# Optimization experiments

Hardware: AMD Instinct MI355X
Metric: run time of the kernel (lower is better)

The kernel has to match this reference:

```python
import jax, jax.numpy as jnp
import numpy as np

N = 4096      # num nodes
E = 131072    # num edges
D = 128       # embed dim (in=out)
HID = 16      # kan hidden dim
G, K = 4, 3   # KAN grid_size / spline_order (GCN + FFN kans)
GA, KA = 2, 1 # attention KANLinear grid_size / spline_order
H, HD = 8, 16 # heads, head_dim

def make_grid(in_f, g, k):
    h = 2.0 / g
    pts = (np.arange(-k, g + k + 1) * h - 1.0).astype(np.float32)  # [g+2k+1]
    return jnp.asarray(np.tile(pts[None, :], (in_f, 1)))            # [in_f, g+2k+1]

GRID_D = make_grid(D, G, K)
GRID_H = make_grid(HID, G, K)
GRID_A = make_grid(D, GA, KA)

def b_splines(x, grid, k):
    # x: [n, in] -> B-spline bases [n, in, g+k] via Cox-de-Boor recursion
    x = x[:, :, None]
    g = grid[None]
    bases = ((x >= g[..., :-1]) & (x < g[..., 1:])).astype(x.dtype)
    for j in range(1, k + 1):
        bases = ((x - g[..., :-(j + 1)]) / (g[..., j:-1] - g[..., :-(j + 1)]) * bases[..., :-1]
                 + (g[..., j + 1:] - x) / (g[..., j + 1:] - g[..., 1:-j]) * bases[..., 1:])
    return bases

def kan_lin(x, bw, sw, grid, k, use_silu):
    base = jax.nn.silu(x) if use_silu else x
    return base @ bw.T + jnp.einsum('nig,oig->no', b_splines(x, grid, k), sw)

def ekan2(x, bw1, sw1, bw2, sw2):
    # eKAN with layers_hidden=[D, HID, D], SiLU base activation
    h = kan_lin(x, bw1, sw1, GRID_D, K, True)
    return kan_lin(h, bw2, sw2, GRID_H, K, True)

def layer_norm(h, s, b):
    m = jnp.mean(h, axis=-1, keepdims=True)
    v = jnp.var(h, axis=-1, keepdims=True)
    return (h - m) * jax.lax.rsqrt(v + 1e-5) * s + b

def setup_inputs() -> dict:
    key = jax.random.key(0)
    ks = jax.random.split(key, 20)
    r = lambda i, shape: jax.random.normal(ks[i], shape, jnp.float32) * 0.1
    return dict(
        x=jax.random.normal(ks[0], (N, D), jnp.float32),
        edge_index=jax.random.randint(ks[1], (2, E), 0, N),
        gcn_bw1=r(2, (HID, D)), gcn_sw1=r(3, (HID, D, G + K)),
        gcn_bw2=r(4, (D, HID)), gcn_sw2=r(5, (D, HID, G + K)),
        q_bw=r(6, (D, D)), q_sw=r(7, (D, D, GA + KA)),
        k_bw=r(8, (D, D)), k_sw=r(9, (D, D, GA + KA)),
        v_bw=r(10, (D, D)), v_sw=r(11, (D, D, GA + KA)),
        ffn_bw1=r(12, (HID, D)), ffn_sw1=r(13, (HID, D, G + K)),
        ffn_bw2=r(14, (D, HID)), ffn_sw2=r(15, (D, HID, G + K)),
        ln1_s=jnp.ones(D), ln1_b=jnp.zeros(D),
        ln2_s=jnp.ones(D), ln2_b=jnp.zeros(D),
        ln3_s=jnp.ones(D), ln3_b=jnp.zeros(D),
    )

def reference(x, edge_index, gcn_bw1, gcn_sw1, gcn_bw2, gcn_sw2,
              q_bw, q_sw, k_bw, k_sw, v_bw, v_sw,
              ffn_bw1, ffn_sw1, ffn_bw2, ffn_sw2,
              ln1_s, ln1_b, ln2_s, ln2_b, ln3_s, ln3_b):
    n = x.shape[0]
    # ---- local GCN-KAN branch: KAN(A_hat x) ----
    loops = jnp.arange(n)
    row = jnp.concatenate([edge_index[0], loops])  # sources (+ self-loops)
    col = jnp.concatenate([edge_index[1], loops])  # targets
    w = jnp.ones(row.shape[0], x.dtype)
    deg = jax.ops.segment_sum(w, row, num_segments=n)
    dis = jnp.where(deg > 0, deg ** -0.5, 0.0)
    norm = dis[row] * w * dis[col]
    agg = jax.ops.segment_sum(norm[:, None] * x[row], col, num_segments=n)  # [n, D]
    h_local = ekan2(agg, gcn_bw1, gcn_sw1, gcn_bw2, gcn_sw2)
    h_local = layer_norm(x + h_local, ln1_s, ln1_b)
    # ---- global KAN multi-head attention branch ----
    Q = kan_lin(x, q_bw, q_sw, GRID_A, KA, False).reshape(n, H, HD)
    Kv = kan_lin(x, k_bw, k_sw, GRID_A, KA, False).reshape(n, H, HD)
    V = kan_lin(x, v_bw, v_sw, GRID_A, KA, False).reshape(n, H, HD)
    scores = jnp.einsum('nhd,mhd->hnm', Q, Kv) / np.sqrt(HD)  # [H, n, n]
    attn = jax.nn.softmax(scores, axis=-1)
    h_attn = jnp.einsum('hnm,mhd->nhd', attn, V).reshape(n, D)
    h_attn = layer_norm(x + h_attn, ln2_s, ln2_b)
    # ---- combine + KAN feed-forward ----
    h = h_local + h_attn
    out = layer_norm(h + ekan2(h, ffn_bw1, ffn_sw1, ffn_bw2, ffn_sw2), ln3_s, ln3_b)
    return out
```

## Files before the change

### kernel.cpp

```cpp
#include <hip/hip_runtime.h>

typedef unsigned short u16;
typedef unsigned int u32;

#define D_ 128
#define HID_ 16
#define NH_ 8
#define HD_ 16
#define PSTRIDE 17

#define WE_W1G 0
#define WE_W2G 16384
#define WE_W1F 32768
#define WE_W2F 49152
#define WE_TOTAL 65536

#define KROW 24
#define VROW 136
#define PROW 40
#define HROW 136
#define AROW 1032
#define HVROW 132

#define QSCALE 0.3606737602222409f

typedef __attribute__((ext_vector_type(8))) short bfrag;
typedef __attribute__((ext_vector_type(4))) float ffrag;

#if defined(__has_builtin)
#if __has_builtin(__builtin_amdgcn_exp2f)
#define EXP2F(x) __builtin_amdgcn_exp2f(x)
#endif
#endif
#ifndef EXP2F
#define EXP2F(x) exp2f(x)
#endif


__device__ __forceinline__ float bf2f(u16 u) {
    union { u32 i; float f; } v; v.i = ((u32)u) << 16; return v.f;
}
__device__ __forceinline__ u16 f2bf(float f) {
    u32 x = __float_as_uint(f);
    u32 r = (x + 0x7fffu + ((x >> 16) & 1u)) >> 16;
    return (u16)r;
}
__device__ __forceinline__ float rdf(const void* p, int i, bool bf) {
    return bf ? bf2f(((const u16*)p)[i]) : ((const float*)p)[i];
}

__device__ __forceinline__ u32 probe_stat(const u16* p) {
    for (int i = 0; i < 128; i++) {
        u16 u = p[i];
        int e = (u >> 7) & 0xFF;
        int m = u & 0x7F;
        bool zero = (e == 0) && (m == 0);
        bool sane = zero || (e >= 97 && e <= 147);
        if (!sane) return 0u;
    }
    return 1u;
}

__global__ __launch_bounds__(256) void k_detect(const void* x,
                         const void* gbw1, const void* gsw1, const void* gbw2, const void* gsw2,
                         const void* qbw, const void* qsw, const void* kbw, const void* ksw,
                         const void* vbw, const void* vsw,
                         const void* fbw1, const void* fsw1, const void* fbw2, const void* fsw2,
                         const void* l1s, const void* l1b, const void* l2s, const void* l2b,
                         const void* l3s, const void* l3b,
                         u32* flags, int* __restrict__ cnt3, int N) {
    int t = threadIdx.x;
    const void* ptrs[21] = {x, gbw1, gsw1, gbw2, gsw2, qbw, qsw, kbw, ksw, vbw, vsw,
                            fbw1, fsw1, fbw2, fsw2, l1s, l1b, l2s, l2b, l3s, l3b};
    if (t < 21) {
        u32 f = 0;
        if (t == 15 || t == 17 || t == 19) {
            f = (((const u32*)ptrs[t])[0] != 0x3F800000u) ? 1u : 0u;
        } else if (t == 16 || t == 18 || t == 20) {
            f = 0;
        } else {
            f = probe_stat((const u16*)ptrs[t]);
        }
        flags[t] = f;
    }
    __syncthreads();
    if (t == 16 || t == 18 || t == 20) flags[t] = flags[t - 1];
    int tot = 3 * N;
    for (int i = t; i < tot; i += 256) cnt3[i] = 0;
}

__device__ __forceinline__ float cub_seg(float s) {
    if (s < 0.0f || s >= 4.0f) return 0.0f;
    if (s < 1.0f) return s * s * s * (1.0f / 6.0f);
    if (s < 2.0f) { float r = s - 1.0f; return (1.0f + 3.0f * r + 3.0f * r * r - 3.0f * r * r * r) * (1.0f / 6.0f); }
    if (s < 3.0f) { float r = s - 2.0f; return (4.0f - 6.0f * r * r + 3.0f * r * r * r) * (1.0f / 6.0f); }
    float q = 4.0f - s; return q * q * q * (1.0f / 6.0f);
}
__device__ __forceinline__ float lin_seg(float s) {
    if (s < 0.0f || s >= 2.0f) return 0.0f;
    return (s < 1.0f) ? s : (2.0f - s);
}

__device__ __forceinline__ uint4 feat8(float a) {
    float si = a / (1.0f + __expf(-a));
    float u = (a + 2.5f) * 2.0f;
    float b0 = cub_seg(u), b1 = cub_seg(u - 1.0f), b2 = cub_seg(u - 2.0f), b3 = cub_seg(u - 3.0f);
    float b4 = cub_seg(u - 4.0f), b5 = cub_seg(u - 5.0f), b6 = cub_seg(u - 6.0f);
    uint4 r;
    r.x = (u32)f2bf(si) | ((u32)f2bf(b0) << 16);
    r.y = (u32)f2bf(b1) | ((u32)f2bf(b2) << 16);
    r.z = (u32)f2bf(b3) | ((u32)f2bf(b4) << 16);
    r.w = (u32)f2bf(b5) | ((u32)f2bf(b6) << 16);
    return r;
}

__global__ __launch_bounds__(256) void k_setup(const void* __restrict__ x,
        const void* l1s, const void* l1b, const void* l2s,
        const void* l2b, const void* l3s, const void* l3b,
        const void* gbw1, const void* gsw1, const void* gbw2, const void* gsw2,
        const void* fbw1, const void* fsw1, const void* fbw2, const void* fsw2,
        const void* qbw, const void* qsw, const void* kbw, const void* ksw,
        const void* vbw, const void* vsw,
        const int* __restrict__ ei,
        const u32* __restrict__ flags,
        float* __restrict__ xin, float* __restrict__ lnp,
        u16* __restrict__ F,
        u16* __restrict__ Web, u16* __restrict__ Wb,
        int* __restrict__ cnt, int* __restrict__ degi,
        int N, int E) {
    int b = blockIdx.x;
    int convB = ((N * D_ + 768) + 255) >> 8;
    if (b < convB) {
        int i = b * 256 + threadIdx.x;
        if (i < N * D_) {
            float xv = rdf(x, i, flags[0] != 0);
            xin[i] = xv;
            float u = xv + 2.0f;
            u32 lo = (u32)f2bf(xv) | ((u32)f2bf(lin_seg(u)) << 16);
            u32 hi = (u32)f2bf(lin_seg(u - 1.0f)) | ((u32)f2bf(lin_seg(u - 2.0f)) << 16);
            ((uint2*)F)[i] = make_uint2(lo, hi);
        } else if (i < N * D_ + 768) {
            int j = i - N * D_;
            int sel = j >> 7, k = j & 127;
            const void* p = sel == 0 ? l1s : sel == 1 ? l1b : sel == 2 ? l2s
                         : sel == 3 ? l2b : sel == 4 ? l3s : l3b;
            lnp[j] = rdf(p, k, flags[15 + sel] != 0);
        }
    } else if (b < convB + 224) {
        int t = (b - convB) * 256 + threadIdx.x;
        if (t < 8192) {
            int seg = t >> 11, i = t & 2047;
            const void* bw = seg == 0 ? gbw1 : seg == 1 ? gbw2 : seg == 2 ? fbw1 : fbw2;
            const void* sw = seg == 0 ? gsw1 : seg == 1 ? gsw2 : seg == 2 ? fsw1 : fsw2;
            int fb = seg == 0 ? 1 : seg == 1 ? 3 : seg == 2 ? 11 : 13;
            bool bwbf = flags[fb] != 0, swbf = flags[fb + 1] != 0;
            u16* dst = Web + (size_t)seg * 16384 + (size_t)i * 8;
            dst[0] = f2bf(rdf(bw, i, bwbf));
#pragma unroll
            for (int g = 0; g < 7; g++) dst[1 + g] = f2bf(rdf(sw, i * 7 + g, swbf));
        } else if (t < 8192 + 49152) {
            int uu = t - 8192;
            int seg = uu >> 14, i = uu & 16383;
            const void* bw = seg == 0 ? qbw : seg == 1 ? kbw : vbw;
            const void* sw = seg == 0 ? qsw : seg == 1 ? ksw : vsw;
            int fb = 5 + seg * 2;
            bool bwbf = flags[fb] != 0, swbf = flags[fb + 1] != 0;
            float sc = (seg == 0) ? QSCALE : 1.0f;
            u16* dst = Wb + (size_t)seg * 65536 + (size_t)i * 4;
            dst[0] = f2bf(rdf(bw, i, bwbf) * sc);
#pragma unroll
            for (int g = 0; g < 3; g++) dst[1 + g] = f2bf(rdf(sw, i * 3 + g, swbf) * sc);
        }
    } else {
        int e = (b - convB - 224) * 256 + threadIdx.x;
        if (e < E) {
            atomicAdd(&degi[ei[e]], 1);
            atomicAdd(&cnt[ei[E + e]], 1);
        }
    }
}

__global__ __launch_bounds__(1024) void k_scan(const int* __restrict__ cnt,
                                               const int* __restrict__ degi,
                                               int* __restrict__ rowptr,
                                               float* __restrict__ dis, int N) {
    __shared__ int ws[16];
    int t = threadIdx.x;
    int base = t * 4;
    int a[4];
#pragma unroll
    for (int k = 0; k < 4; k++) a[k] = (base + k < N) ? cnt[base + k] : 0;
    int loc = a[0] + a[1] + a[2] + a[3];
    int pre = loc;
#pragma unroll
    for (int off = 1; off < 64; off <<= 1) {
        int v = __shfl_up(pre, off, 64);
        if ((t & 63) >= off) pre += v;
    }
    if ((t & 63) == 63) ws[t >> 6] = pre;
    __syncthreads();
    if (t < 64) {
        int v = (t < 16) ? ws[t] : 0;
#pragma unroll
        for (int off = 1; off < 16; off <<= 1) {
            int u = __shfl_up(v, off, 64);
            if (t >= off) v += u;
        }
        if (t < 16) ws[t] = v;
    }
    __syncthreads();
    int ex = pre - loc + ((t >= 64) ? ws[(t >> 6) - 1] : 0);
    int run = ex;
#pragma unroll
    for (int k = 0; k < 4; k++) {
        if (base + k < N) rowptr[base + k] = run;
        run += a[k];
    }
    if (t == 1023) rowptr[N] = ws[15];
#pragma unroll
    for (int k = 0; k < 4; k++)
        if (base + k < N) dis[base + k] = rsqrtf((float)degi[base + k] + 1.0f);
}

__global__ void k_fill(const int* __restrict__ ei, const int* __restrict__ rowptr,
                       int* __restrict__ fill, int* __restrict__ elist, int E) {
    int e = blockIdx.x * 256 + threadIdx.x;
    if (e < E) {
        int r = ei[e], c = ei[E + e];
        int pos = rowptr[c] + atomicAdd(&fill[c], 1);
        elist[pos] = r;
    }
}

#define EKAN_G1(W1B) \
    if (ww == 0) { \
        const u16* ar = hfA + (size_t)l15 * AROW + quad * 8; \
        const u16* br = (W1B) + (size_t)l15 * 1024 + quad * 8; \
        ffrag c0 = {0,0,0,0}, c1 = {0,0,0,0}, c2 = {0,0,0,0}, c3 = {0,0,0,0}; \
        for (int ks = 0; ks < 256; ks += 32) { \
            c0 = __builtin_amdgcn_mfma_f32_16x16x32_bf16(*(const bfrag*)(ar + ks),       *(const bfrag*)(br + ks),       c0, 0, 0, 0); \
            c1 = __builtin_amdgcn_mfma_f32_16x16x32_bf16(*(const bfrag*)(ar + 256 + ks), *(const bfrag*)(br + 256 + ks), c1, 0, 0, 0); \
            c2 = __builtin_amdgcn_mfma_f32_16x16x32_bf16(*(const bfrag*)(ar + 512 + ks), *(const bfrag*)(br + 512 + ks), c2, 0, 0, 0); \
            c3 = __builtin_amdgcn_mfma_f32_16x16x32_bf16(*(const bfrag*)(ar + 768 + ks), *(const bfrag*)(br + 768 + ks), c3, 0, 0, 0); \
        } \
        float e0 = (c0.x + c1.x) + (c2.x + c3.x); \
        float e1 = (c0.y + c1.y) + (c2.y + c3.y); \
        float e2 = (c0.z + c1.z) + (c2.z + c3.z); \
        float e3 = (c0.w + c1.w) + (c2.w + c3.w); \
        { uint4 fv = feat8(e0); *(uint4*)(&hfL[(quad * 4 + 0) * HROW + l15 * 8]) = fv; } \
        { uint4 fv = feat8(e1); *(uint4*)(&hfL[(quad * 4 + 1) * HROW + l15 * 8]) = fv; } \
        { uint4 fv = feat8(e2); *(uint4*)(&hfL[(quad * 4 + 2) * HROW + l15 * 8]) = fv; } \
        { uint4 fv = feat8(e3); *(uint4*)(&hfL[(quad * 4 + 3) * HROW + l15 * 8]) = fv; } \
    }

#define EK_TGET(RR, COMP, V0, V1, RES0EXPR, RES1EXPR) { \
    int row = quad * 4 + RR; \
    float r0 = (RES0EXPR); \
    float r1 = (RES1EXPR); \
    V0 = a0.COMP + r0; V1 = a1.COMP + r1; \
    float s1 = V0 + V1, s2 = V0 * V0 + V1 * V1; \
    s1 += __shfl_xor(s1, 1, 64); s2 += __shfl_xor(s2, 1, 64); \
    s1 += __shfl_xor(s1, 2, 64); s2 += __shfl_xor(s2, 2, 64); \
    s1 += __shfl_xor(s1, 4, 64); s2 += __shfl_xor(s2, 4, 64); \
    s1 += __shfl_xor(s1, 8, 64); s2 += __shfl_xor(s2, 8, 64); \
    if (l15 == 0) { redS[ww * 16 + row] = s1; redS[64 + ww * 16 + row] = s2; } }

#define EK_TOUT(RR, V0, V1, OUTP, BFO) { \
    int row = quad * 4 + RR; \
    float s1 = (redS[row] + redS[16 + row]) + (redS[32 + row] + redS[48 + row]); \
    float s2 = (redS[64 + row] + redS[80 + row]) + (redS[96 + row] + redS[112 + row]); \
    float mean = s1 * 0.0078125f; \
    float var = s2 * 0.0078125f - mean * mean; \
    float rs = rsqrtf(var + 1e-5f); \
    float y0 = (V0 - mean) * rs * ls0 + lb0; \
    float y1 = (V1 - mean) * rs * ls1 + lb1; \
    int node = node0 + row; \
    if (BFO) { \
        u16* ob = (u16*)(OUTP) + (size_t)node * 128; \
        ob[c0i] = f2bf(y0); ob[c1i] = f2bf(y1); \
    } else { \
        float* ob = (float*)(OUTP) + (size_t)node * 128; \
        ob[c0i] = y0; ob[c1i] = y1; \
    } }

#define EKAN_G2LN(W2B, LNS, LNB, RES0EXPR, RES1EXPR, OUTP, BFO) { \
    const u16* b0 = (W2B) + (size_t)l15 * 128 + quad * 8 + (size_t)(2 * ww) * 2048; \
    ffrag a0 = {0,0,0,0}, a1 = {0,0,0,0}; \
    for (int ks = 0; ks < 128; ks += 32) { \
        bfrag af = *(const bfrag*)(&hfL[l15 * HROW + quad * 8 + ks]); \
        a0 = __builtin_amdgcn_mfma_f32_16x16x32_bf16(af, *(const bfrag*)(b0 + ks),        a0, 0, 0, 0); \
        a1 = __builtin_amdgcn_mfma_f32_16x16x32_bf16(af, *(const bfrag*)(b0 + 2048 + ks), a1, 0, 0, 0); \
    } \
    int c0i = 32 * ww + l15, c1i = c0i + 16; \
    float ls0 = (LNS)[c0i], lb0 = (LNB)[c0i]; \
    float ls1 = (LNS)[c1i], lb1 = (LNB)[c1i]; \
    float v0r0, v0r1, v0r2, v0r3, v1r0, v1r1, v1r2, v1r3; \
    EK_TGET(0, x, v0r0, v1r0, RES0EXPR, RES1EXPR) \
    EK_TGET(1, y, v0r1, v1r1, RES0EXPR, RES1EXPR) \
    EK_TGET(2, z, v0r2, v1r2, RES0EXPR, RES1EXPR) \
    EK_TGET(3, w, v0r3, v1r3, RES0EXPR, RES1EXPR) \
    __syncthreads(); \
    EK_TOUT(0, v0r0, v1r0, OUTP, BFO) \
    EK_TOUT(1, v0r1, v1r1, OUTP, BFO) \
    EK_TOUT(2, v0r2, v1r2, OUTP, BFO) \
    EK_TOUT(3, v0r3, v1r3, OUTP, BFO) }

__global__ __launch_bounds__(256) void k_gcn_ekan(
        const int* __restrict__ rowptr, const int* __restrict__ elist,
        const float* __restrict__ dis, const float* __restrict__ xin,
        const u16* __restrict__ W1b, const u16* __restrict__ W2b,
        const float* __restrict__ lns, const float* __restrict__ lnb,
        float* __restrict__ hl, int N) {
    __shared__ u16 hfA[16 * AROW];
    __shared__ u16 hfL[16 * HROW];
    __shared__ float redS[128];
    __shared__ int idsH[2][128];
    __shared__ float wshH[2][128];
    int mt = blockIdx.x, t = threadIdx.x;
    int half = t >> 7, d = t & 127;
    int ww = t >> 6, lane = t & 63, quad = lane >> 4, l15 = lane & 15;
    int node0 = mt * 16;
#pragma unroll 1
    for (int i = 0; i < 16; i += 2) {
        int nodeA = node0 + i, nodeB = node0 + i + 1;
        int begA = rowptr[nodeA], endA = rowptr[nodeA + 1];
        int begB = rowptr[nodeB], endB = rowptr[nodeB + 1];
        int tripsA = (endA - begA + 127) >> 7;
        int tripsB = (endB - begB + 127) >> 7;
        int trips = max(tripsA, tripsB);
        int beg = half ? begB : begA;
        int end = half ? endB : endA;
        float acc = 0.0f, acc2 = 0.0f;
        for (int tr = 0; tr < trips; tr++) {
            int j0 = beg + (tr << 7);
            int cc = min(128, end - j0);
            __syncthreads();
            if (d < cc) {
                int rr = elist[j0 + d];
                idsH[half][d] = rr;
                wshH[half][d] = dis[rr];
            }
            __syncthreads();
            int j = 0;
            for (; j + 2 <= cc; j += 2) {
                acc  += wshH[half][j]     * xin[(size_t)idsH[half][j]     * D_ + d];
                acc2 += wshH[half][j + 1] * xin[(size_t)idsH[half][j + 1] * D_ + d];
            }
            if (j < cc) acc += wshH[half][j] * xin[(size_t)idsH[half][j] * D_ + d];
        }
        int node = half ? nodeB : nodeA;
        float dc = dis[node];
        float a = dc * (acc + acc2 + dc * xin[(size_t)node * D_ + d]);
        *(uint4*)(&hfA[(i + half) * AROW + d * 8]) = feat8(a);
    }
    __syncthreads();
    EKAN_G1(W1b)
    __syncthreads();
    EKAN_G2LN(W2b, lns, lnb,
              xin[(size_t)(node0 + row) * 128 + c0i],
              xin[(size_t)(node0 + row) * 128 + c1i],
              hl, false)
    (void)lane;
}

#define QKV_STORE(ACC, TL) { \
    int col = cg * 48 + (TL) * 16 + l15; \
    int mat = col >> 7, idx = col & 127; \
    u16* dstb = (mat == 0) ? Qb : (mat == 1) ? Kb : Vb; \
    size_t base = (size_t)(idx >> 4) * N * HD_ + (size_t)(idx & 15); \
    dstb[base + (size_t)(rowb + 0) * HD_] = f2bf(ACC.x); \
    dstb[base + (size_t)(rowb + 1) * HD_] = f2bf(ACC.y); \
    dstb[base + (size_t)(rowb + 2) * HD_] = f2bf(ACC.z); \
    dstb[base + (size_t)(rowb + 3) * HD_] = f2bf(ACC.w); \
}

__global__ __launch_bounds__(64) void k_qkv5(const u16* __restrict__ F,
        const u16* __restrict__ Wb,
        u16* __restrict__ Qb, u16* __restrict__ Kb, u16* __restrict__ Vb, int N) {
    int mt = blockIdx.x, cg = blockIdx.y;
    int lane = threadIdx.x, quad = lane >> 4, l15 = lane & 15;
    const u16* arow = F + (size_t)(mt * 16 + l15) * 512 + quad * 8;
    const u16* b0r = Wb + (size_t)(cg * 48 + l15) * 512 + quad * 8;
    const u16* b1r = b0r + 16 * 512;
    const u16* b2r = b0r + 32 * 512;
    ffrag a0 = {0, 0, 0, 0}, a1 = {0, 0, 0, 0}, a2 = {0, 0, 0, 0};
#pragma unroll
    for (int ks = 0; ks < 512; ks += 32) {
        bfrag af = *(const bfrag*)(arow + ks);
        bfrag bf0 = *(const bfrag*)(b0r + ks);
        bfrag bf1 = *(const bfrag*)(b1r + ks);
        bfrag bf2 = *(const bfrag*)(b2r + ks);
        a0 = __builtin_amdgcn_mfma_f32_16x16x32_bf16(af, bf0, a0, 0, 0, 0);
        a1 = __builtin_amdgcn_mfma_f32_16x16x32_bf16(af, bf1, a1, 0, 0, 0);
        a2 = __builtin_amdgcn_mfma_f32_16x16x32_bf16(af, bf2, a2, 0, 0, 0);
    }
    int rowb = mt * 16 + quad * 4;
    QKV_STORE(a0, 0)
    QKV_STORE(a1, 1)
    QKV_STORE(a2, 2)
}

#define ATTN_SCORE(QF, LACC, PBT) { \
    ffrag zz = {0.0f, 0.0f, 0.0f, 0.0f}; \
    ffrag s0 = __builtin_amdgcn_mfma_f32_16x16x32_bf16(QF, kf0, zz, 0, 0, 0); \
    ffrag s1 = __builtin_amdgcn_mfma_f32_16x16x32_bf16(QF, kf1, zz, 0, 0, 0); \
    float a0 = EXP2F(s0.x), a1 = EXP2F(s0.y), a2 = EXP2F(s0.z), a3 = EXP2F(s0.w); \
    float b0 = EXP2F(s1.x), b1 = EXP2F(s1.y), b2 = EXP2F(s1.z), b3 = EXP2F(s1.w); \
    LACC.x += a0 + b0; LACC.y += a1 + b1; LACC.z += a2 + b2; LACC.w += a3 + b3; \
    u32* pw = (u32*)PBT; \
    pw[(quad * 4 + 0) * (PROW / 2) + l15] = (__float_as_uint(a0) >> 16) | (__float_as_uint(b0) & 0xFFFF0000u); \
    pw[(quad * 4 + 1) * (PROW / 2) + l15] = (__float_as_uint(a1) >> 16) | (__float_as_uint(b1) & 0xFFFF0000u); \
    pw[(quad * 4 + 2) * (PROW / 2) + l15] = (__float_as_uint(a2) >> 16) | (__float_as_uint(b2) & 0xFFFF0000u); \
    pw[(quad * 4 + 3) * (PROW / 2) + l15] = (__float_as_uint(a3) >> 16) | (__float_as_uint(b3) & 0xFFFF0000u); \
}

#define ATTN_PV(OACC, PBT) { \
    bfrag pf = *(const bfrag*)(&PBT[l15 * PROW + quad * 8]); \
    OACC = __builtin_amdgcn_mfma_f32_16x16x32_bf16(pf, vf, OACC, 0, 0, 0); \
}

#define STORE_TILE(OACC, LACC, TL) { \
    int q0 = qtb + (TL) * 16 + quad * 4; \
    float* pp; \
    pp = part + ((size_t)(h * N + q0 + 0) * SPLIT + s) * PSTRIDE; \
    pp[1 + l15] = OACC.x; if (l15 == 0) pp[0] = LACC.x; \
    pp = part + ((size_t)(h * N + q0 + 1) * SPLIT + s) * PSTRIDE; \
    pp[1 + l15] = OACC.y; if (l15 == 0) pp[0] = LACC.y; \
    pp = part + ((size_t)(h * N + q0 + 2) * SPLIT + s) * PSTRIDE; \
    pp[1 + l15] = OACC.z; if (l15 == 0) pp[0] = LACC.z; \
    pp = part + ((size_t)(h * N + q0 + 3) * SPLIT + s) * PSTRIDE; \
    pp[1 + l15] = OACC.w; if (l15 == 0) pp[0] = LACC.w; \
}

__global__ __launch_bounds__(256) void k_attn9(const u16* __restrict__ Qb,
        const u16* __restrict__ Kb, const u16* __restrict__ Vb,
        float* __restrict__ part, int N, int SPLIT) {
    int s = blockIdx.x, qb = blockIdx.y, h = blockIdx.z;
    int t = threadIdx.x;
    int w = t >> 6, lane = t & 63, quad = lane >> 4, l15 = lane & 15;
    __shared__ u16 ldsK[128 * KROW + 16];
    __shared__ u16 ldsVt[16 * VROW];
    __shared__ u16 ldsP[4][4][16 * PROW];

    const u16* qrow = Qb + (size_t)h * N * HD_;
    const u16* krow = Kb + (size_t)h * N * HD_;
    const u16* vrow = Vb + (size_t)h * N * HD_;

    for (int i = t; i < (128 * KROW + 16) / 2; i += 256) ((u32*)ldsK)[i] = 0;

    int qtb = qb * 256 + w * 64;
    bfrag qz = {0, 0, 0, 0, 0, 0, 0, 0};
    bfrag qf0 = qz, qf1 = qz, qf2 = qz, qf3 = qz;
    if (quad < 2) {
        qf0 = *(const bfrag*)(qrow + (size_t)(qtb + 0 * 16 + l15) * HD_ + quad * 8);
        qf1 = *(const bfrag*)(qrow + (size_t)(qtb + 1 * 16 + l15) * HD_ + quad * 8);
        qf2 = *(const bfrag*)(qrow + (size_t)(qtb + 2 * 16 + l15) * HD_ + quad * 8);
        qf3 = *(const bfrag*)(qrow + (size_t)(qtb + 3 * 16 + l15) * HD_ + quad * 8);
    }

    ffrag o0 = {0, 0, 0, 0}, o1 = {0, 0, 0, 0}, o2 = {0, 0, 0, 0}, o3 = {0, 0, 0, 0};
    ffrag L0 = {0, 0, 0, 0}, L1 = {0, 0, 0, 0}, L2 = {0, 0, 0, 0}, L3 = {0, 0, 0, 0};
    u16* pb0 = &ldsP[w][0][0];
    u16* pb1 = &ldsP[w][1][0];
    u16* pb2 = &ldsP[w][2][0];
    u16* pb3 = &ldsP[w][3][0];

    int keys = N / SPLIT;
    int kstart0 = s * keys;
    for (int kst = 0; kst < keys; kst += 128) {
        int kg = kstart0 + kst;
        __syncthreads();
        if (t < 128) {
            const uint4* src = (const uint4*)(krow + (size_t)(kg + t) * HD_);
            uint4 a = src[0], b = src[1];
            *(uint4*)(&ldsK[t * KROW]) = a;
            *(uint4*)(&ldsK[t * KROW + 8]) = b;
        } else {
            int key = t - 128;
            const uint4* src = (const uint4*)(vrow + (size_t)(kg + key) * HD_);
            uint4 a = src[0], b = src[1];
            ldsVt[0 * VROW + key] = (u16)(a.x);  ldsVt[1 * VROW + key] = (u16)(a.x >> 16);
            ldsVt[2 * VROW + key] = (u16)(a.y);  ldsVt[3 * VROW + key] = (u16)(a.y >> 16);
            ldsVt[4 * VROW + key] = (u16)(a.z);  ldsVt[5 * VROW + key] = (u16)(a.z >> 16);
            ldsVt[6 * VROW + key] = (u16)(a.w);  ldsVt[7 * VROW + key] = (u16)(a.w >> 16);
            ldsVt[8 * VROW + key] = (u16)(b.x);  ldsVt[9 * VROW + key] = (u16)(b.x >> 16);
            ldsVt[10 * VROW + key] = (u16)(b.y); ldsVt[11 * VROW + key] = (u16)(b.y >> 16);
            ldsVt[12 * VROW + key] = (u16)(b.z); ldsVt[13 * VROW + key] = (u16)(b.z >> 16);
            ldsVt[14 * VROW + key] = (u16)(b.w); ldsVt[15 * VROW + key] = (u16)(b.w >> 16);
        }
        __syncthreads();
#pragma unroll
        for (int koff = 0; koff < 128; koff += 32) {
            bfrag kf0 = *(const bfrag*)(&ldsK[(koff + 2 * l15) * KROW + quad * 8]);
            bfrag kf1 = *(const bfrag*)(&ldsK[(koff + 2 * l15 + 1) * KROW + quad * 8]);
            bfrag vf = *(const bfrag*)(&ldsVt[l15 * VROW + koff + quad * 8]);
            ATTN_SCORE(qf0, L0, pb0)
            ATTN_SCORE(qf1, L1, pb1)
            ATTN_SCORE(qf2, L2, pb2)
            ATTN_SCORE(qf3, L3, pb3)
            __asm__ volatile("s_waitcnt lgkmcnt(0)" ::: "memory");
            ATTN_PV(o0, pb0)
            ATTN_PV(o1, pb1)
            ATTN_PV(o2, pb2)
            ATTN_PV(o3, pb3)
        }
    }

#pragma unroll
    for (int off = 1; off < 16; off <<= 1) {
        L0.x += __shfl_xor(L0.x, off, 64); L0.y += __shfl_xor(L0.y, off, 64);
        L0.z += __shfl_xor(L0.z, off, 64); L0.w += __shfl_xor(L0.w, off, 64);
        L1.x += __shfl_xor(L1.x, off, 64); L1.y += __shfl_xor(L1.y, off, 64);
        L1.z += __shfl_xor(L1.z, off, 64); L1.w += __shfl_xor(L1.w, off, 64);
        L2.x += __shfl_xor(L2.x, off, 64); L2.y += __shfl_xor(L2.y, off, 64);
        L2.z += __shfl_xor(L2.z, off, 64); L2.w += __shfl_xor(L2.w, off, 64);
        L3.x += __shfl_xor(L3.x, off, 64); L3.y += __shfl_xor(L3.y, off, 64);
        L3.z += __shfl_xor(L3.z, off, 64); L3.w += __shfl_xor(L3.w, off, 64);
    }
    STORE_TILE(o0, L0, 0)
    STORE_TILE(o1, L1, 1)
    STORE_TILE(o2, L2, 2)
    STORE_TILE(o3, L3, 3)
}

__global__ __launch_bounds__(256) void k_comb_ekan(
        const float* __restrict__ part,
        const float* __restrict__ xin, const float* __restrict__ hl,
        const float* __restrict__ lnp,
        const u16* __restrict__ W1b, const u16* __restrict__ W2b,
        void* __restrict__ outp, const u32* __restrict__ flags,
        int N, int SPLIT) {
    __shared__ u16 hfA[16 * AROW];
    __shared__ u16 hfL[16 * HROW];
    __shared__ float redS[128];
    __shared__ float hvL[16 * HVROW];
    __shared__ float redA[4], redB[4];
    int mt = blockIdx.x, t = threadIdx.x;
    int half = t >> 7, tl = t & 127;
    int ww = t >> 6, lane = t & 63, quad = lane >> 4, l15 = lane & 15;
    int hh = tl >> 4, dd = tl & 15;
    int node0 = mt * 16;
#pragma unroll 1
    for (int i = 0; i < 16; i += 2) {
        int node = node0 + i + half;
        float L = 0.0f, O = 0.0f;
        for (int ss = 0; ss < SPLIT; ss++) {
            const float* ps = part + ((size_t)(hh * N + node) * SPLIT + ss) * PSTRIDE;
            L += ps[0];
            O += ps[1 + dd];
        }
        float r = xin[(size_t)node * D_ + tl] + O / L;
        float s1 = r, s2 = r * r;
#pragma unroll
        for (int off = 1; off < 64; off <<= 1) {
            s1 += __shfl_xor(s1, off, 64);
            s2 += __shfl_xor(s2, off, 64);
        }
        if ((t & 63) == 0) { redA[ww] = s1; redB[ww] = s2; }
        __syncthreads();
        float S1 = redA[half * 2] + redA[half * 2 + 1];
        float S2 = redB[half * 2] + redB[half * 2 + 1];
        float mean = S1 * 0.0078125f;
        float var = S2 * 0.0078125f - mean * mean;
        float rs = rsqrtf(var + 1e-5f);
        float y2 = (r - mean) * rs * lnp[256 + tl] + lnp[384 + tl];
        float hvv = hl[(size_t)node * D_ + tl] + y2;
        hvL[(i + half) * HVROW + tl] = hvv;
        *(uint4*)(&hfA[(i + half) * AROW + tl * 8]) = feat8(hvv);
        __syncthreads();
    }
    bool bfo = flags[0] != 0;
    EKAN_G1(W1b)
    __syncthreads();
    EKAN_G2LN(W2b, lnp + 512, lnp + 640,
              hvL[row * HVROW + c0i],
              hvL[row * HVROW + c1i],
              outp, bfo)
    (void)lane;
}

extern "C" void kernel_launch(void* const* d_in, const int* in_sizes, int n_in,
                              void* d_out, int out_size, void* d_ws, size_t ws_size,
                              hipStream_t stream) {
    const void* x = d_in[0];
    const int* ei = (const int*)d_in[1];
    const void* gbw1 = d_in[2];
    const void* gsw1 = d_in[3];
    const void* gbw2 = d_in[4];
    const void* gsw2 = d_in[5];
    const void* qbw = d_in[6];
    const void* qsw = d_in[7];
    const void* kbw = d_in[8];
    const void* ksw = d_in[9];
    const void* vbw = d_in[10];
    const void* vsw = d_in[11];
    const void* fbw1 = d_in[12];
    const void* fsw1 = d_in[13];
    const void* fbw2 = d_in[14];
    const void* fsw2 = d_in[15];
    const void* ln1s = d_in[16];
    const void* ln1b = d_in[17];
    const void* ln2s = d_in[18];
    const void* ln2b = d_in[19];
    const void* ln3s = d_in[20];
    const void* ln3b = d_in[21];

    const int N = in_sizes[0] / D_;
    const int E = in_sizes[1] / 2;
    const size_t ND = (size_t)N * D_;

    float* wf = (float*)d_ws;
    u32* flags = (u32*)wf;
    float* lnp = wf + 32;
    float* dis = wf + 800;
    float* xin = dis + N;
    float* hl  = xin + ND;
    u16* Web = (u16*)(hl + ND);
    u16* Wb  = Web + WE_TOTAL;
    u16* F   = Wb + 196608;
    u16* Qb  = F + (size_t)N * 512;
    u16* Kb  = Qb + ND;
    u16* Vb  = Kb + ND;
    int* cnt    = (int*)(Vb + ND);
    int* fill   = cnt + N;
    int* degi   = fill + N;
    int* rowptr = degi + N;
    int* elist  = rowptr + N + 1;
    float* part = (float*)(elist + E);

    size_t baseBytes = (size_t)((char*)part - (char*)d_ws);
    int SPLIT = 8;
    if (baseBytes + (size_t)NH_ * N * 8 * PSTRIDE * 4 > ws_size) SPLIT = 4;
    if (baseBytes + (size_t)NH_ * N * 4 * PSTRIDE * 4 > ws_size) SPLIT = 2;

    int convB = ((N * D_ + 768) + 255) >> 8;
    int countB = (E + 255) / 256;

    k_detect<<<1, 256, 0, stream>>>(x, gbw1, gsw1, gbw2, gsw2, qbw, qsw, kbw, ksw,
                                    vbw, vsw, fbw1, fsw1, fbw2, fsw2,
                                    ln1s, ln1b, ln2s, ln2b, ln3s, ln3b, flags, cnt, N);
    k_setup<<<convB + 224 + countB, 256, 0, stream>>>(
        x, ln1s, ln1b, ln2s, ln2b, ln3s, ln3b,
        gbw1, gsw1, gbw2, gsw2, fbw1, fsw1, fbw2, fsw2,
        qbw, qsw, kbw, ksw, vbw, vsw,
        ei, flags, xin, lnp, F, Web, Wb, cnt, degi, N, E);
    k_qkv5<<<dim3(N / 16, 8), 64, 0, stream>>>(F, Wb, Qb, Kb, Vb, N);
    k_scan<<<1, 1024, 0, stream>>>(cnt, degi, rowptr, dis, N);
    k_fill<<<countB, 256, 0, stream>>>(ei, rowptr, fill, elist, E);
    k_gcn_ekan<<<N / 16, 256, 0, stream>>>(rowptr, elist, dis, xin,
                                           Web + WE_W1G, Web + WE_W2G,
                                           lnp + 0, lnp + 128, hl, N);
    k_attn9<<<dim3(SPLIT, N / 256, NH_), 256, 0, stream>>>(Qb, Kb, Vb, part, N, SPLIT);
    k_comb_ekan<<<N / 16, 256, 0, stream>>>(part, xin, hl, lnp,
                                            Web + WE_W1F, Web + WE_W2F,
                                            d_out, flags, N, SPLIT);
}
```

Before: 283.5 us.

## Split GCN aggregation into per-node kernel and separate eKAN kernel

Moves the neighbor aggregation out of the fused GCN+eKAN kernel into its own kernel with one 128-thread block per node and four independent accumulators. The bf16 spline features go through a global buffer, and a new eKAN kernel reads them directly from global memory in its first GEMM. The aim is more parallelism for the irregular gather, which was serialized over 16 nodes per block before. The cost is an extra launch and a round trip through global memory for an 8x-expanded feature buffer (N*1024 bf16).

After: 249.2 us. -12.1%, faster.

```diff
diff --git a/kernel.cpp b/kernel.cpp
--- a/kernel.cpp
+++ b/kernel.cpp
@@ -232,9 +232,40 @@
     }
 }
 
-#define EKAN_G1(W1B) \
+__global__ __launch_bounds__(128) void k_gcn(const int* __restrict__ rowptr,
+        const int* __restrict__ elist, const float* __restrict__ dis,
+        const float* __restrict__ xin, u16* __restrict__ Afeat) {
+    int c = blockIdx.x, t = threadIdx.x;
+    __shared__ int ids[128];
+    __shared__ float wsh[128];
+    int beg = rowptr[c], end = rowptr[c + 1];
+    float a0 = 0.0f, a1 = 0.0f, a2 = 0.0f, a3 = 0.0f;
+    for (int j0 = beg; j0 < end; j0 += 128) {
+        int cc = min(128, end - j0);
+        __syncthreads();
+        if (t < cc) {
+            int rr = elist[j0 + t];
+            ids[t] = rr;
+            wsh[t] = dis[rr];
+        }
+        __syncthreads();
+        int j = 0;
+        for (; j + 4 <= cc; j += 4) {
+            a0 += wsh[j]     * xin[(size_t)ids[j]     * D_ + t];
+            a1 += wsh[j + 1] * xin[(size_t)ids[j + 1] * D_ + t];
+            a2 += wsh[j + 2] * xin[(size_t)ids[j + 2] * D_ + t];
+            a3 += wsh[j + 3] * xin[(size_t)ids[j + 3] * D_ + t];
+        }
+        for (; j < cc; j++) a0 += wsh[j] * xin[(size_t)ids[j] * D_ + t];
+    }
+    float dc = dis[c];
+    float a = dc * (((a0 + a1) + (a2 + a3)) + dc * xin[(size_t)c * D_ + t]);
+    ((uint4*)Afeat)[(size_t)c * D_ + t] = feat8(a);
+}
+
+#define EKAN_G1(APTR, ASTR, W1B) \
     if (ww == 0) { \
-        const u16* ar = hfA + (size_t)l15 * AROW + quad * 8; \
+        const u16* ar = (APTR) + (size_t)l15 * (ASTR) + quad * 8; \
         const u16* br = (W1B) + (size_t)l15 * 1024 + quad * 8; \
         ffrag c0 = {0,0,0,0}, c1 = {0,0,0,0}, c2 = {0,0,0,0}, c3 = {0,0,0,0}; \
         for (int ks = 0; ks < 256; ks += 32) { \
@@ -305,61 +336,23 @@
     EK_TOUT(2, v0r2, v1r2, OUTP, BFO) \
     EK_TOUT(3, v0r3, v1r3, OUTP, BFO) }
 
-__global__ __launch_bounds__(256) void k_gcn_ekan(
-        const int* __restrict__ rowptr, const int* __restrict__ elist,
-        const float* __restrict__ dis, const float* __restrict__ xin,
+__global__ __launch_bounds__(256) void k_ekan4(const u16* __restrict__ A,
         const u16* __restrict__ W1b, const u16* __restrict__ W2b,
+        const float* __restrict__ resid,
         const float* __restrict__ lns, const float* __restrict__ lnb,
-        float* __restrict__ hl, int N) {
-    __shared__ u16 hfA[16 * AROW];
+        float* __restrict__ outp, int N) {
     __shared__ u16 hfL[16 * HROW];
     __shared__ float redS[128];
-    __shared__ int idsH[2][128];
-    __shared__ float wshH[2][128];
     int mt = blockIdx.x, t = threadIdx.x;
-    int half = t >> 7, d = t & 127;
     int ww = t >> 6, lane = t & 63, quad = lane >> 4, l15 = lane & 15;
     int node0 = mt * 16;
-#pragma unroll 1
-    for (int i = 0; i < 16; i += 2) {
-        int nodeA = node0 + i, nodeB = node0 + i + 1;
-        int begA = rowptr[nodeA], endA = rowptr[nodeA + 1];
-        int begB = rowptr[nodeB], endB = rowptr[nodeB + 1];
-        int tripsA = (endA - begA + 127) >> 7;
-        int tripsB = (endB - begB + 127) >> 7;
-        int trips = max(tripsA, tripsB);
-        int beg = half ? begB : begA;
-        int end = half ? endB : endA;
-        float acc = 0.0f, acc2 = 0.0f;
-        for (int tr = 0; tr < trips; tr++) {
-            int j0 = beg + (tr << 7);
-            int cc = min(128, end - j0);
-            __syncthreads();
-            if (d < cc) {
-                int rr = elist[j0 + d];
-                idsH[half][d] = rr;
-                wshH[half][d] = dis[rr];
-            }
-            __syncthreads();
-            int j = 0;
-            for (; j + 2 <= cc; j += 2) {
-                acc  += wshH[half][j]     * xin[(size_t)idsH[half][j]     * D_ + d];
-                acc2 += wshH[half][j + 1] * xin[(size_t)idsH[half][j + 1] * D_ + d];
-            }
-            if (j < cc) acc += wshH[half][j] * xin[(size_t)idsH[half][j] * D_ + d];
-        }
-        int node = half ? nodeB : nodeA;
-        float dc = dis[node];
-        float a = dc * (acc + acc2 + dc * xin[(size_t)node * D_ + d]);
-        *(uint4*)(&hfA[(i + half) * AROW + d * 8]) = feat8(a);
-    }
-    __syncthreads();
-    EKAN_G1(W1b)
+    const u16* Ab = A + (size_t)node0 * 1024;
+    EKAN_G1(Ab, 1024, W1b)
     __syncthreads();
     EKAN_G2LN(W2b, lns, lnb,
-              xin[(size_t)(node0 + row) * 128 + c0i],
-              xin[(size_t)(node0 + row) * 128 + c1i],
-              hl, false)
+              resid[(size_t)(node0 + row) * 128 + c0i],
+              resid[(size_t)(node0 + row) * 128 + c1i],
+              outp, false)
     (void)lane;
 }
 
@@ -570,7 +563,7 @@
         __syncthreads();
     }
     bool bfo = flags[0] != 0;
-    EKAN_G1(W1b)
+    EKAN_G1(hfA, AROW, W1b)
     __syncthreads();
     EKAN_G2LN(W2b, lnp + 512, lnp + 640,
               hvL[row * HVROW + c0i],
@@ -621,7 +614,8 @@
     u16* Qb  = F + (size_t)N * 512;
     u16* Kb  = Qb + ND;
     u16* Vb  = Kb + ND;
-    int* cnt    = (int*)(Vb + ND);
+    u16* Afeat = Vb + ND;
+    int* cnt    = (int*)(Afeat + (size_t)N * 1024);
     int* fill   = cnt + N;
     int* degi   = fill + N;
     int* rowptr = degi + N;
@@ -647,9 +641,9 @@
     k_qkv5<<<dim3(N / 16, 8), 64, 0, stream>>>(F, Wb, Qb, Kb, Vb, N);
     k_scan<<<1, 1024, 0, stream>>>(cnt, degi, rowptr, dis, N);
     k_fill<<<countB, 256, 0, stream>>>(ei, rowptr, fill, elist, E);
-    k_gcn_ekan<<<N / 16, 256, 0, stream>>>(rowptr, elist, dis, xin,
-                                           Web + WE_W1G, Web + WE_W2G,
-                                           lnp + 0, lnp + 128, hl, N);
+    k_gcn<<<N, 128, 0, stream>>>(rowptr, elist, dis, xin, Afeat);
+    k_ekan4<<<N / 16, 256, 0, stream>>>(Afeat, Web + WE_W1G, Web + WE_W2G, xin,
+                                        lnp + 0, lnp + 128, hl, N);
     k_attn9<<<dim3(SPLIT, N / 256, NH_), 256, 0, stream>>>(Qb, Kb, Vb, part, N, SPLIT);
     k_comb_ekan<<<N / 16, 256, 0, stream>>>(part, xin, hl, lnp,
                                             Web + WE_W1F, Web + WE_W2F,
```
